# Kernel tuning notes

Measured on AMD Instinct MI355X. Metric: run time of the kernel, lower is better.

## Reference

```python
import jax, jax.numpy as jnp
import numpy as np

NUM_TOPICS = 100
VOCAB = 8192
MC_N = 20
MD_N = 20
LAMBDA_D = 0.7
LAMBDA_A = 100.0
WARMUP_RATIO = 0.5
NUM_EPOCHS = 200


def setup_inputs() -> dict:
    key = jax.random.key(0)
    k1, k2 = jax.random.split(key)
    beta = jax.random.normal(k1, (NUM_TOPICS, VOCAB), dtype=jnp.float32)
    W = jax.random.uniform(k2, (VOCAB, VOCAB), dtype=jnp.float32)
    # fill_diagonal_(1) in __init__
    d = jnp.arange(VOCAB)
    W = W.at[d, d].set(1.0)
    return {"beta": beta, "coherence_weight": W, "epoch": 120}


def reference(beta, coherence_weight, epoch):
    K, V = beta.shape
    rows = jnp.arange(K)[:, None]

    # --- Mc: top-Mc_n mask -> additive -99999 on non-topk entries ---
    _, mc_idx = jax.lax.top_k(beta, MC_N)                      # [K, Mc_n]
    Mc = jnp.zeros_like(beta).at[rows, mc_idx].set(1.0)        # [K, V]
    Mc_add = (1.0 - Mc) * (-99999.0)

    # softmax over masked beta is detached in the original
    p = jax.lax.stop_gradient(jax.nn.softmax(beta + Mc_add, axis=1))
    M = p @ coherence_weight                                    # [K, V]

    # row-wise min-max normalize, then Wc = 1 - normalized
    m_min = jnp.min(M, axis=1, keepdims=True)
    m_max = jnp.max(M, axis=1, keepdims=True)
    Wc = 1.0 - (M - m_min) / (m_max - m_min)

    loss = 100.0 * jax.nn.softmax(beta, axis=1) ** 2 * Wc       # [K, V]

    # --- diversity mask Md (lambda_d > 0.5 branch) ---
    _, md_idx = jax.lax.top_k(beta, MD_N)
    Md_mask = jnp.zeros_like(beta).at[rows, md_idx].set(1.0)    # [K, V]
    # Md[t, v] = any other row has v in its top-Md_n
    col_sum = jnp.sum(Md_mask, axis=0)                          # [V]
    Md = (col_sum[None, :] - Md_mask) > 0                       # [K, V] bool

    pos = jnp.sum(jnp.where(Md, loss, 0.0))
    neg = jnp.sum(jnp.where(Md, 0.0, loss))
    total = (pos * LAMBDA_D + neg * (1.0 - LAMBDA_D)) * 2.0

    warmup_epochs = int(WARMUP_RATIO * NUM_EPOCHS)              # 100
    lambda_a_delta = LAMBDA_A / warmup_epochs
    lambda_a = epoch * lambda_a_delta if epoch < warmup_epochs else LAMBDA_A
    return lambda_a * total
```

## Files before the change

### kernel.cpp

```cpp
#include <hip/hip_runtime.h>
#include <math.h>

#define NT 100
#define VOCAB 8192
#define TOPN 20
#define CHUNKS 8
#define CCOLS 1024
#define NB (NT * CHUNKS)
#define CAP 2048
#define NWV 16
#define PRE (NWV * TOPN)

__global__ __launch_bounds__(1024) void topk_kernel(
    const float* __restrict__ beta,
    int*   __restrict__ top_idx,
    float* __restrict__ top_p,
    float* __restrict__ rowstats)
{
    const int k = blockIdx.x;
    const int t = threadIdx.x;
    const int wv = t >> 6;
    const int lane = t & 63;

    __shared__ float sred[NWV];
    __shared__ int   sredi[NWV];
    __shared__ int   s_base;
    __shared__ float cu[CAP];
    __shared__ int   ci[CAP];
    __shared__ float pv[PRE];
    __shared__ int   pi[PRE];
    __shared__ float s_winv[TOPN];
    __shared__ int   s_wini[TOPN];
    __shared__ float s_ps;

    const float* row = beta + (size_t)k * VOCAB;
    float4 r0 = *reinterpret_cast<const float4*>(row + (size_t)t * 4);
    float4 r1 = *reinterpret_cast<const float4*>(row + (size_t)(1024 + t) * 4);

    float mx = fmaxf(fmaxf(fmaxf(r0.x, r0.y), fmaxf(r0.z, r0.w)),
                     fmaxf(fmaxf(r1.x, r1.y), fmaxf(r1.z, r1.w)));
#pragma unroll
    for (int off = 32; off >= 1; off >>= 1) mx = fmaxf(mx, __shfl_down(mx, off));
    if (lane == 0) sred[wv] = mx;
    __syncthreads();
    float rowmax = sred[0];
#pragma unroll
    for (int w = 1; w < NWV; ++w) rowmax = fmaxf(rowmax, sred[w]);
    __syncthreads();

    float T = rowmax - 2.0f;
    for (int guard = 0; guard < 64; ++guard) {
        int c = 0;
        c += (r0.x >= T) + (r0.y >= T) + (r0.z >= T) + (r0.w >= T);
        c += (r1.x >= T) + (r1.y >= T) + (r1.z >= T) + (r1.w >= T);
#pragma unroll
        for (int off = 32; off >= 1; off >>= 1) c += __shfl_down(c, off);
        if (lane == 0) sredi[wv] = c;
        __syncthreads();
        int cnt = 0;
#pragma unroll
        for (int w = 0; w < NWV; ++w) cnt += sredi[w];
        if (cnt >= TOPN) break;
        T -= 0.5f;
        __syncthreads();
    }
    if (t == 0) s_base = 0;
    __syncthreads();

#pragma unroll
    for (int i = 0; i < 2; ++i) {
        const float4 rr = (i == 0) ? r0 : r1;
#pragma unroll
        for (int e = 0; e < 4; ++e) {
            const float v = (&rr.x)[e];
            const int idx = (i * 1024 + t) * 4 + e;
            const bool pr = (v >= T);
            const unsigned long long mask = __ballot(pr);
            const int pre = __popcll(mask & ((1ull << lane) - 1ull));
            int base = 0;
            if (lane == 0) base = atomicAdd(&s_base, __popcll(mask));
            base = __shfl(base, 0);
            if (pr) {
                const int p = base + pre;
                if (p < CAP) { cu[p] = v; ci[p] = idx; }
            }
        }
    }
    __syncthreads();
    const int ncand = min(s_base, CAP);

    {
        const int seg = (ncand + NWV - 1) / NWV;
        const int lo = wv * seg;
        const int hi = min(lo + seg, ncand);
        for (int it = 0; it < TOPN; ++it) {
            float bv = -INFINITY; int bp = -1;
            for (int p = lo + lane; p < hi; p += 64) {
                const float v = cu[p];
                if (v > bv) { bv = v; bp = p; }
            }
#pragma unroll
            for (int off = 32; off >= 1; off >>= 1) {
                const float ov = __shfl_down(bv, off);
                const int   op = __shfl_down(bp, off);
                if (ov > bv) { bv = ov; bp = op; }
            }
            bp = __shfl(bp, 0);
            bv = __shfl(bv, 0);
            if (lane == 0) {
                pv[wv * TOPN + it] = bv;
                pi[wv * TOPN + it] = (bp >= 0) ? ci[bp] : 0;
            }
            if (bp >= 0) cu[bp] = -INFINITY;
        }
    }
    __syncthreads();

    if (wv == 0) {
        for (int it = 0; it < TOPN; ++it) {
            float bv = -INFINITY; int bp = -1;
#pragma unroll
            for (int rp = 0; rp < PRE / 64; ++rp) {
                const int p = rp * 64 + lane;
                const float v = pv[p];
                if (v > bv) { bv = v; bp = p; }
            }
#pragma unroll
            for (int off = 32; off >= 1; off >>= 1) {
                const float ov = __shfl_down(bv, off);
                const int   op = __shfl_down(bp, off);
                if (ov > bv) { bv = ov; bp = op; }
            }
            bp = __shfl(bp, 0);
            bv = __shfl(bv, 0);
            if (lane == 0) { s_winv[it] = bv; s_wini[it] = pi[bp]; }
            pv[bp] = -INFINITY;
        }
    }
    __syncthreads();

    if (t == 0) {
        float ps = 0.f;
#pragma unroll
        for (int j = 0; j < TOPN; ++j) ps += expf(s_winv[j] - rowmax);
        s_ps = ps;
    }
    __syncthreads();
    if (t < TOPN) {
        top_idx[k * TOPN + t] = s_wini[t];
        top_p[k * TOPN + t]   = expf(s_winv[t] - rowmax) / s_ps;
    }

    float se = expf(r0.x - rowmax) + expf(r0.y - rowmax)
             + expf(r0.z - rowmax) + expf(r0.w - rowmax)
             + expf(r1.x - rowmax) + expf(r1.y - rowmax)
             + expf(r1.z - rowmax) + expf(r1.w - rowmax);
#pragma unroll
    for (int off = 32; off >= 1; off >>= 1) se += __shfl_down(se, off);
    if (lane == 0) sred[wv] = se;
    __syncthreads();
    if (t == 0) {
        float s = 0.f;
#pragma unroll
        for (int w = 0; w < NWV; ++w) s += sred[w];
        rowstats[2 * k + 0] = rowmax;
        rowstats[2 * k + 1] = s;
    }
}

__global__ __launch_bounds__(256) void fused_kernel(
    const float* __restrict__ beta,
    const float* __restrict__ W,
    const int*   __restrict__ top_idx,
    const float* __restrict__ top_p,
    const float* __restrict__ rowstats,
    float* __restrict__ part6)
{
    const int b = blockIdx.x;
    const int k = b / CHUNKS;
    const int c = b % CHUNKS;
    const int t = threadIdx.x;

    __shared__ int   sIdx[TOPN];
    __shared__ float sP[TOPN];
    __shared__ int   cnt[CCOLS];
    __shared__ float sA[4], sB[4], sC[4], sD[4], sE[4], sF[4];

    if (t < TOPN) { sIdx[t] = top_idx[k * TOPN + t]; sP[t] = top_p[k * TOPN + t]; }
#pragma unroll
    for (int i = 0; i < CCOLS / 256; ++i) cnt[i * 256 + t] = 0;
    __syncthreads();

    int   idx_r[TOPN];
    float p_r[TOPN];
#pragma unroll
    for (int j = 0; j < TOPN; ++j) { idx_r[j] = sIdx[j]; p_r[j] = sP[j]; }

    const int lo  = c * CCOLS;
    const int col = lo + t * 4;
    float4 w_r[TOPN];
#pragma unroll
    for (int j = 0; j < TOPN; ++j)
        w_r[j] = *reinterpret_cast<const float4*>(W + (size_t)idx_r[j] * VOCAB + col);
    const float4 bv = *reinterpret_cast<const float4*>(beta + (size_t)k * VOCAB + col);

#pragma unroll 8
    for (int e = t; e < NT * TOPN; e += 256) {
        const int v = top_idx[e] - lo;
        if ((unsigned)v < (unsigned)CCOLS) atomicAdd(&cnt[v], 1);
    }
    __syncthreads();
    if (t < TOPN) {
        const int v = sIdx[t] - lo;
        if ((unsigned)v < (unsigned)CCOLS) atomicSub(&cnt[v], 1);
    }

    float4 m = make_float4(0.f, 0.f, 0.f, 0.f);
#pragma unroll
    for (int j = 0; j < TOPN; ++j) {
        const float pj = p_r[j];
        m.x += pj * w_r[j].x; m.y += pj * w_r[j].y;
        m.z += pj * w_r[j].z; m.w += pj * w_r[j].w;
    }

    float mn  = fminf(fminf(m.x, m.y), fminf(m.z, m.w));
    float mxv = fmaxf(fmaxf(m.x, m.y), fmaxf(m.z, m.w));

    const float rmax = rowstats[2 * k + 0];
    const float rinv = 1.0f / rowstats[2 * k + 1];
    float4 w4;
    w4.x = expf(bv.x - rmax) * rinv;  w4.x = 100.f * w4.x * w4.x;
    w4.y = expf(bv.y - rmax) * rinv;  w4.y = 100.f * w4.y * w4.y;
    w4.z = expf(bv.z - rmax) * rinv;  w4.z = 100.f * w4.z * w4.z;
    w4.w = expf(bv.w - rmax) * rinv;  w4.w = 100.f * w4.w * w4.w;

    __syncthreads();

    float Apos = 0.f, Bpos = 0.f, Aneg = 0.f, Bneg = 0.f;
    {
        const int lc = t * 4;
        if (cnt[lc + 0] > 0) { Apos += w4.x; Bpos += w4.x * m.x; } else { Aneg += w4.x; Bneg += w4.x * m.x; }
        if (cnt[lc + 1] > 0) { Apos += w4.y; Bpos += w4.y * m.y; } else { Aneg += w4.y; Bneg += w4.y * m.y; }
        if (cnt[lc + 2] > 0) { Apos += w4.z; Bpos += w4.z * m.z; } else { Aneg += w4.z; Bneg += w4.z * m.z; }
        if (cnt[lc + 3] > 0) { Apos += w4.w; Bpos += w4.w * m.w; } else { Aneg += w4.w; Bneg += w4.w * m.w; }
    }

#pragma unroll
    for (int off = 32; off >= 1; off >>= 1) {
        mn   = fminf(mn,  __shfl_down(mn,  off));
        mxv  = fmaxf(mxv, __shfl_down(mxv, off));
        Apos += __shfl_down(Apos, off);
        Bpos += __shfl_down(Bpos, off);
        Aneg += __shfl_down(Aneg, off);
        Bneg += __shfl_down(Bneg, off);
    }
    if ((t & 63) == 0) {
        const int w = t >> 6;
        sA[w] = mn; sB[w] = mxv; sC[w] = Apos; sD[w] = Bpos; sE[w] = Aneg; sF[w] = Bneg;
    }
    __syncthreads();
    if (t == 0) {
        part6[b * 6 + 0] = fminf(fminf(sA[0], sA[1]), fminf(sA[2], sA[3]));
        part6[b * 6 + 1] = fmaxf(fmaxf(sB[0], sB[1]), fmaxf(sB[2], sB[3]));
        part6[b * 6 + 2] = sC[0] + sC[1] + sC[2] + sC[3];
        part6[b * 6 + 3] = sD[0] + sD[1] + sD[2] + sD[3];
        part6[b * 6 + 4] = sE[0] + sE[1] + sE[2] + sE[3];
        part6[b * 6 + 5] = sF[0] + sF[1] + sF[2] + sF[3];
    }
}

__global__ __launch_bounds__(128) void finalize_kernel(
    const float* __restrict__ part6,
    const int*   __restrict__ epoch,
    float* __restrict__ out)
{
    const int t = threadIdx.x;
    __shared__ float sp[128], sn[128];
    float pos = 0.f, neg = 0.f;
    if (t < NT) {
        float mn = INFINITY, mxv = -INFINITY;
        float Ap = 0.f, Bp = 0.f, An = 0.f, Bn = 0.f;
        for (int cc = 0; cc < CHUNKS; ++cc) {
            const float* p6 = part6 + (size_t)(t * CHUNKS + cc) * 6;
            mn  = fminf(mn,  p6[0]);
            mxv = fmaxf(mxv, p6[1]);
            Ap += p6[2]; Bp += p6[3]; An += p6[4]; Bn += p6[5];
        }
        const float inv = 1.0f / (mxv - mn);
        pos = Ap - inv * (Bp - mn * Ap);
        neg = An - inv * (Bn - mn * An);
    }
    sp[t] = pos; sn[t] = neg;
    __syncthreads();
    if (t == 0) {
        float P = 0.f, N = 0.f;
        for (int i = 0; i < NT; ++i) { P += sp[i]; N += sn[i]; }
        const float total = (P * 0.7f + N * 0.3f) * 2.0f;
        const int e = *epoch;
        const float la = (e < 100) ? (float)e : 100.0f;
        *out = la * total;
    }
}

extern "C" void kernel_launch(void* const* d_in, const int* in_sizes, int n_in,
                              void* d_out, int out_size, void* d_ws, size_t ws_size,
                              hipStream_t stream)
{
    (void)in_sizes; (void)n_in; (void)out_size; (void)ws_size;
    const float* beta  = (const float*)d_in[0];
    const float* W     = (const float*)d_in[1];
    const int*   epoch = (const int*)d_in[2];
    float* out = (float*)d_out;

    char* ws = (char*)d_ws;
    int*   top_idx  = (int*)ws;    ws += NT * TOPN * sizeof(int);
    float* top_p    = (float*)ws;  ws += NT * TOPN * sizeof(float);
    float* rowstats = (float*)ws;  ws += NT * 2 * sizeof(float);
    float* part6    = (float*)ws;  ws += NB * 6 * sizeof(float);

    topk_kernel<<<NT, 1024, 0, stream>>>(beta, top_idx, top_p, rowstats);
    fused_kernel<<<NB, 256, 0, stream>>>(beta, W, top_idx, top_p, rowstats, part6);
    finalize_kernel<<<1, 128, 0, stream>>>(part6, epoch, out);
}
```

Measured before the change: 51.06 us.

## Restructure top-k kernel into per-wavefront independent selection with 256 threads

The top-k kernel now runs 256 threads per row. Each wavefront owns a 2048-column slice and computes its own max, sum-exp, adaptive threshold and candidate list without block-level barriers or shared atomics. A single merge step combines the per-wave top-20 results and rescales the per-wave softmax sums, using the top winner as the row max. This removes most __syncthreads and atomic traffic in the selection phase. In exchange, each wave does more serial work, and candidates are capped at 256 per wave with a bounded threshold search.

```diff
diff --git a/kernel.cpp b/kernel.cpp
--- a/kernel.cpp
+++ b/kernel.cpp
@@ -4,14 +4,14 @@
 #define NT 100
 #define VOCAB 8192
 #define TOPN 20
+#define NWV 4
+#define WCOLS 2048
+#define SCAP 256
 #define CHUNKS 8
 #define CCOLS 1024
 #define NB (NT * CHUNKS)
-#define CAP 2048
-#define NWV 16
-#define PRE (NWV * TOPN)
-
-__global__ __launch_bounds__(1024) void topk_kernel(
+
+__global__ __launch_bounds__(256) void topk_kernel(
     const float* __restrict__ beta,
     int*   __restrict__ top_idx,
     float* __restrict__ top_p,
@@ -22,81 +22,100 @@
     const int wv = t >> 6;
     const int lane = t & 63;
 
-    __shared__ float sred[NWV];
-    __shared__ int   sredi[NWV];
-    __shared__ int   s_base;
-    __shared__ float cu[CAP];
-    __shared__ int   ci[CAP];
-    __shared__ float pv[PRE];
-    __shared__ int   pi[PRE];
+    __shared__ float cu[NWV * SCAP];
+    __shared__ int   cid[NWV * SCAP];
+    __shared__ float smaxs[NWV], ssums[NWV];
+    __shared__ float pv[NWV * TOPN];
+    __shared__ int   pid[NWV * TOPN];
     __shared__ float s_winv[TOPN];
     __shared__ int   s_wini[TOPN];
-    __shared__ float s_ps;
-
-    const float* row = beta + (size_t)k * VOCAB;
-    float4 r0 = *reinterpret_cast<const float4*>(row + (size_t)t * 4);
-    float4 r1 = *reinterpret_cast<const float4*>(row + (size_t)(1024 + t) * 4);
-
-    float mx = fmaxf(fmaxf(fmaxf(r0.x, r0.y), fmaxf(r0.z, r0.w)),
-                     fmaxf(fmaxf(r1.x, r1.y), fmaxf(r1.z, r1.w)));
-#pragma unroll
-    for (int off = 32; off >= 1; off >>= 1) mx = fmaxf(mx, __shfl_down(mx, off));
-    if (lane == 0) sred[wv] = mx;
-    __syncthreads();
-    float rowmax = sred[0];
-#pragma unroll
-    for (int w = 1; w < NWV; ++w) rowmax = fmaxf(rowmax, sred[w]);
-    __syncthreads();
-
-    float T = rowmax - 2.0f;
-    for (int guard = 0; guard < 64; ++guard) {
+    __shared__ float s_ps, s_rowmax;
+
+    const float* base = beta + (size_t)k * VOCAB + wv * WCOLS;
+    float4 r[8];
+    float mx = -INFINITY;
+#pragma unroll
+    for (int i = 0; i < 8; ++i) {
+        r[i] = *reinterpret_cast<const float4*>(base + (size_t)(i * 64 + lane) * 4);
+        mx = fmaxf(mx, fmaxf(fmaxf(r[i].x, r[i].y), fmaxf(r[i].z, r[i].w)));
+    }
+#pragma unroll
+    for (int off = 32; off >= 1; off >>= 1) mx = fmaxf(mx, __shfl_xor(mx, off));
+    const float smax = mx;
+
+    float se = 0.f;
+#pragma unroll
+    for (int i = 0; i < 8; ++i) {
+        se += expf(r[i].x - smax) + expf(r[i].y - smax)
+            + expf(r[i].z - smax) + expf(r[i].w - smax);
+    }
+#pragma unroll
+    for (int off = 32; off >= 1; off >>= 1) se += __shfl_xor(se, off);
+    const float ssum = se;
+
+    if (lane == 0) { smaxs[wv] = smax; ssums[wv] = ssum; }
+
+    float T = smax - 1.5f;
+    for (int g = 0; g < 16; ++g) {
         int c = 0;
-        c += (r0.x >= T) + (r0.y >= T) + (r0.z >= T) + (r0.w >= T);
-        c += (r1.x >= T) + (r1.y >= T) + (r1.z >= T) + (r1.w >= T);
-#pragma unroll
-        for (int off = 32; off >= 1; off >>= 1) c += __shfl_down(c, off);
-        if (lane == 0) sredi[wv] = c;
-        __syncthreads();
-        int cnt = 0;
-#pragma unroll
-        for (int w = 0; w < NWV; ++w) cnt += sredi[w];
-        if (cnt >= TOPN) break;
-        T -= 0.5f;
-        __syncthreads();
-    }
-    if (t == 0) s_base = 0;
-    __syncthreads();
-
-#pragma unroll
-    for (int i = 0; i < 2; ++i) {
-        const float4 rr = (i == 0) ? r0 : r1;
+#pragma unroll
+        for (int i = 0; i < 8; ++i) {
+            c += (r[i].x >= T) + (r[i].y >= T) + (r[i].z >= T) + (r[i].w >= T);
+        }
+#pragma unroll
+        for (int off = 32; off >= 1; off >>= 1) c += __shfl_xor(c, off);
+        if (c >= TOPN) break;
+        T -= 0.4f;
+    }
+
+    int wbase = 0;
+#pragma unroll
+    for (int i = 0; i < 8; ++i) {
 #pragma unroll
         for (int e = 0; e < 4; ++e) {
-            const float v = (&rr.x)[e];
-            const int idx = (i * 1024 + t) * 4 + e;
+            const float v = (&r[i].x)[e];
             const bool pr = (v >= T);
             const unsigned long long mask = __ballot(pr);
             const int pre = __popcll(mask & ((1ull << lane) - 1ull));
-            int base = 0;
-            if (lane == 0) base = atomicAdd(&s_base, __popcll(mask));
-            base = __shfl(base, 0);
             if (pr) {
-                const int p = base + pre;
-                if (p < CAP) { cu[p] = v; ci[p] = idx; }
+                const int p = wbase + pre;
+                if (p < SCAP) {
+                    cu[wv * SCAP + p]  = v;
+                    cid[wv * SCAP + p] = wv * WCOLS + (i * 64 + lane) * 4 + e;
+                }
             }
-        }
-    }
-    __syncthreads();
-    const int ncand = min(s_base, CAP);
-
-    {
-        const int seg = (ncand + NWV - 1) / NWV;
-        const int lo = wv * seg;
-        const int hi = min(lo + seg, ncand);
+            wbase += __popcll(mask);
+        }
+    }
+    const int n = min(wbase, SCAP);
+
+    for (int it = 0; it < TOPN; ++it) {
+        float bv = -INFINITY; int bp = -1;
+        for (int p = lane; p < n; p += 64) {
+            const float v = cu[wv * SCAP + p];
+            if (v > bv) { bv = v; bp = p; }
+        }
+#pragma unroll
+        for (int off = 32; off >= 1; off >>= 1) {
+            const float ov = __shfl_down(bv, off);
+            const int   op = __shfl_down(bp, off);
+            if (ov > bv) { bv = ov; bp = op; }
+        }
+        bp = __shfl(bp, 0);
+        bv = __shfl(bv, 0);
+        if (lane == 0) {
+            pv[wv * TOPN + it]  = bv;
+            pid[wv * TOPN + it] = (bp >= 0) ? cid[wv * SCAP + bp] : 0;
+        }
+        if (bp >= 0) cu[wv * SCAP + bp] = -INFINITY;
+    }
+    __syncthreads();
+
+    if (wv == 0) {
         for (int it = 0; it < TOPN; ++it) {
             float bv = -INFINITY; int bp = -1;
-            for (int p = lo + lane; p < hi; p += 64) {
-                const float v = cu[p];
+            for (int p = lane; p < NWV * TOPN; p += 64) {
+                const float v = pv[p];
                 if (v > bv) { bv = v; bp = p; }
             }
 #pragma unroll
@@ -107,64 +126,27 @@
             }
             bp = __shfl(bp, 0);
             bv = __shfl(bv, 0);
-            if (lane == 0) {
-                pv[wv * TOPN + it] = bv;
-                pi[wv * TOPN + it] = (bp >= 0) ? ci[bp] : 0;
-            }
-            if (bp >= 0) cu[bp] = -INFINITY;
-        }
-    }
-    __syncthreads();
-
-    if (wv == 0) {
-        for (int it = 0; it < TOPN; ++it) {
-            float bv = -INFINITY; int bp = -1;
-#pragma unroll
-            for (int rp = 0; rp < PRE / 64; ++rp) {
-                const int p = rp * 64 + lane;
-                const float v = pv[p];
-                if (v > bv) { bv = v; bp = p; }
-            }
-#pragma unroll
-            for (int off = 32; off >= 1; off >>= 1) {
-                const float ov = __shfl_down(bv, off);
-                const int   op = __shfl_down(bp, off);
-                if (ov > bv) { bv = ov; bp = op; }
-            }
-            bp = __shfl(bp, 0);
-            bv = __shfl(bv, 0);
-            if (lane == 0) { s_winv[it] = bv; s_wini[it] = pi[bp]; }
+            if (lane == 0) { s_winv[it] = bv; s_wini[it] = pid[bp]; }
             pv[bp] = -INFINITY;
         }
-    }
-    __syncthreads();
-
-    if (t == 0) {
-        float ps = 0.f;
-#pragma unroll
-        for (int j = 0; j < TOPN; ++j) ps += expf(s_winv[j] - rowmax);
-        s_ps = ps;
+        if (lane == 0) {
+            const float rowmax = s_winv[0];
+            float ps = 0.f;
+#pragma unroll
+            for (int j = 0; j < TOPN; ++j) ps += expf(s_winv[j] - rowmax);
+            float rs = 0.f;
+#pragma unroll
+            for (int s = 0; s < NWV; ++s) rs += ssums[s] * expf(smaxs[s] - rowmax);
+            s_rowmax = rowmax;
+            s_ps = ps;
+            rowstats[2 * k + 0] = rowmax;
+            rowstats[2 * k + 1] = rs;
+        }
     }
     __syncthreads();
     if (t < TOPN) {
         top_idx[k * TOPN + t] = s_wini[t];
-        top_p[k * TOPN + t]   = expf(s_winv[t] - rowmax) / s_ps;
-    }
-
-    float se = expf(r0.x - rowmax) + expf(r0.y - rowmax)
-             + expf(r0.z - rowmax) + expf(r0.w - rowmax)
-             + expf(r1.x - rowmax) + expf(r1.y - rowmax)
-             + expf(r1.z - rowmax) + expf(r1.w - rowmax);
-#pragma unroll
-    for (int off = 32; off >= 1; off >>= 1) se += __shfl_down(se, off);
-    if (lane == 0) sred[wv] = se;
-    __syncthreads();
-    if (t == 0) {
-        float s = 0.f;
-#pragma unroll
-        for (int w = 0; w < NWV; ++w) s += sred[w];
-        rowstats[2 * k + 0] = rowmax;
-        rowstats[2 * k + 1] = s;
+        top_p[k * TOPN + t]   = expf(s_winv[t] - s_rowmax) / s_ps;
     }
 }
 
@@ -318,7 +300,7 @@
     float* rowstats = (float*)ws;  ws += NT * 2 * sizeof(float);
     float* part6    = (float*)ws;  ws += NB * 6 * sizeof(float);
 
-    topk_kernel<<<NT, 1024, 0, stream>>>(beta, top_idx, top_p, rowstats);
+    topk_kernel<<<NT, 256, 0, stream>>>(beta, top_idx, top_p, rowstats);
     fused_kernel<<<NB, 256, 0, stream>>>(beta, W, top_idx, top_p, rowstats, part6);
     finalize_kernel<<<1, 128, 0, stream>>>(part6, epoch, out);
 }
```

Measured after the change: 47.09 us. 7.8% less time.
